# Kernel tuning notes

Measured on AMD Instinct MI355X. Metric: run time of the kernel, lower is better.

## Reference

```python
import jax, jax.numpy as jnp
import numpy as np

B, S, D = 16, 2048, 64
K, M = 8, 2048

def setup_inputs() -> dict:
    key = jax.random.key(0)
    kx, kc = jax.random.split(key)
    x = jax.random.normal(kx, (B, S, D), dtype=jnp.float32)
    # nn.init.uniform_(weight, -1/M, 1/M)
    codebooks = jax.random.uniform(kc, (K, M, D), dtype=jnp.float32,
                                   minval=-1.0 / M, maxval=1.0 / M)
    return {"x": x, "codebooks": codebooks}

def reference(x, codebooks):
    """Residual VQ: sequentially quantize residual against K codebooks.

    x: (B,S,D) float32; codebooks: (K,M,D) float32.
    Returns (quantized (B,S,D), indices (K,B,S) int32).
    Uses squared-distance expansion ||r||^2 - 2 r.c + ||c||^2 (argmin-equivalent
    to torch.norm) to avoid materializing the (B,S,M,D) difference tensor.
    """
    def step(residual, cb):  # residual: (B,S,D), cb: (M,D)
        r2 = jnp.sum(residual * residual, axis=-1, keepdims=True)   # (B,S,1)
        c2 = jnp.sum(cb * cb, axis=-1)                              # (M,)
        cross = jnp.einsum('bsd,md->bsm', residual, cb)             # (B,S,M)
        d2 = r2 - 2.0 * cross + c2                                  # (B,S,M)
        idx = jnp.argmin(d2, axis=-1)                               # (B,S)
        q = cb[idx]                                                 # (B,S,D) gather
        return residual - q, idx

    residual, indices = jax.lax.scan(step, x, codebooks)
    quantized = x - residual
    return quantized, indices
```

## Files before the change

kernel.cpp:

```cpp
#include <hip/hip_runtime.h>


#define BB 16
#define SS 2048
#define DD 64
#define KK 8
#define MM 2048
#define NPTS (BB * SS)
#define QSIZE (NPTS * DD)
#define NCHUNK 8
#define WPB 8
#define PPB 512
#define MCHUNK (MM / NCHUNK)
#define PACKF 16640

__global__ __launch_bounds__(256) void rvq_prep(const float* __restrict__ cb,
                                                float* __restrict__ pack,
                                                unsigned long long* __restrict__ keys) {
#pragma clang fp contract(off)
    const int b = blockIdx.x;
    const int tid = threadIdx.x;
    const float* src = cb + (size_t)b * 16384;
    float* dst = pack + (size_t)b * PACKF;
    for (int i = tid; i < 4096; i += 256)
        *(float4*)&dst[i * 4] = *(const float4*)&src[i * 4];
    const float* row = src + (size_t)tid * DD;
    float r[8];
#pragma unroll
    for (int j = 0; j < 8; ++j) { float v = row[j]; r[j] = v * v; }
#pragma unroll
    for (int i = 8; i < DD; i += 8) {
#pragma unroll
        for (int j = 0; j < 8; ++j) { float v = row[i + j]; float t = v * v; r[j] += t; }
    }
    dst[16384 + tid] = ((r[0] + r[1]) + (r[2] + r[3])) + ((r[4] + r[5]) + (r[6] + r[7]));
    keys[b * 512 + tid] = ~0ULL;
    keys[b * 512 + 256 + tid] = ~0ULL;
}

#define R2K(A, B, C, E) \
    "v_pk_mul_f32 v[92:93], v[" A "], v[" A "]\n\t" \
    "v_pk_add_f32 v[80:81], v[80:81], v[92:93]\n\t" \
    "v_pk_mul_f32 v[92:93], v[" B "], v[" B "]\n\t" \
    "v_pk_add_f32 v[82:83], v[82:83], v[92:93]\n\t" \
    "v_pk_mul_f32 v[92:93], v[" C "], v[" C "]\n\t" \
    "v_pk_add_f32 v[84:85], v[84:85], v[92:93]\n\t" \
    "v_pk_mul_f32 v[92:93], v[" E "], v[" E "]\n\t" \
    "v_pk_add_f32 v[86:87], v[86:87], v[92:93]\n\t"

#define GRP(SA, SB, VA, VB) \
    "v_pk_mul_f32 v[84:85], s[" SA "], v[" VA "]\n\t" \
    "v_pk_mul_f32 v[86:87], s[" SB "], v[" VB "]\n\t" \
    "v_pk_add_f32 v[80:81], v[80:81], v[84:85]\n\t" \
    "v_pk_add_f32 v[82:83], v[82:83], v[86:87]\n\t"

#define GRPL(CA, CB, VA, VB) \
    "v_pk_mul_f32 v[84:85], v[" CA "], v[" VA "]\n\t" \
    "v_pk_mul_f32 v[86:87], v[" CB "], v[" VB "]\n\t" \
    "v_pk_add_f32 v[80:81], v[80:81], v[84:85]\n\t" \
    "v_pk_add_f32 v[82:83], v[82:83], v[86:87]\n\t"

#define SMEM_B_ISSUE \
    "s_add_u32 s15, s14, 0x100\n\t" \
    "s_load_dwordx16 s[16:31], %[pb], s15\n\t" \
    "s_add_u32 s15, s15, 0x40\n\t" \
    "s_load_dwordx16 s[80:95], %[pb], s15\n\t"

#define C2_ISSUE \
    "s_lshr_b32 s15, s14, 6\n\t" \
    "s_add_u32 s15, s15, 0x10008\n\t" \
    "s_min_u32 s15, s15, 0x103f8\n\t" \
    "s_load_dwordx2 s[12:13], %[pb], s15\n\t"

#define SMEM_A_NEXT \
    "s_add_u32 s15, s14, 0x200\n\t" \
    "s_min_u32 s15, s15, 0xfe00\n\t" \
    "s_load_dwordx16 s[32:47], %[pb], s15\n\t" \
    "s_add_u32 s15, s15, 0x40\n\t" \
    "s_load_dwordx16 s[48:63], %[pb], s15\n\t" \
    "s_add_u32 s15, s15, 0x40\n\t" \
    "s_load_dwordx16 s[64:79], %[pb], s15\n\t"

#define EINSM_A \
    "v_pk_mul_f32 v[80:81], s[44:45], v[28:29]\n\t" \
    "v_pk_mul_f32 v[82:83], s[46:47], v[30:31]\n\t" \
    GRP("40:41","42:43","24:25","26:27") \
    GRP("36:37","38:39","20:21","22:23") \
    GRP("32:33","34:35","16:17","18:19") \
    GRP("60:61","62:63","44:45","46:47") \
    GRP("56:57","58:59","40:41","42:43") \
    GRP("52:53","54:55","36:37","38:39") \
    GRP("48:49","50:51","32:33","34:35") \
    GRP("76:77","78:79","60:61","62:63") \
    GRP("72:73","74:75","56:57","58:59") \
    GRP("68:69","70:71","52:53","54:55") \
    GRP("64:65","66:67","48:49","50:51")

#define TAIL_A \
    GRPL("108:109","110:111","76:77","78:79") \
    GRPL("104:105","106:107","72:73","74:75") \
    GRPL("100:101","102:103","68:69","70:71") \
    GRPL("96:97","98:99","64:65","66:67")

#define DS_B \
    "ds_read_b128 v[96:99],   v94 offset:64\n\t" \
    "ds_read_b128 v[100:103], v94 offset:80\n\t" \
    "ds_read_b128 v[104:107], v94 offset:96\n\t" \
    "ds_read_b128 v[108:111], v94 offset:112\n\t" \
    "ds_read_b128 v[112:115], v94 offset:128\n\t" \
    "ds_read_b128 v[116:119], v94 offset:144\n\t" \
    "ds_read_b128 v[120:123], v94 offset:160\n\t" \
    "ds_read_b128 v[124:127], v94 offset:176\n\t"

#define EINSM_B \
    "v_pk_mul_f32 v[80:81], s[28:29], v[28:29]\n\t" \
    "v_pk_mul_f32 v[82:83], s[30:31], v[30:31]\n\t" \
    GRP("24:25","26:27","24:25","26:27") \
    GRP("20:21","22:23","20:21","22:23") \
    GRP("16:17","18:19","16:17","18:19") \
    GRP("92:93","94:95","44:45","46:47") \
    GRP("88:89","90:91","40:41","42:43") \
    GRP("84:85","86:87","36:37","38:39") \
    GRP("80:81","82:83","32:33","34:35")

#define B_B32_THEN_DSA \
    GRPL("108:109","110:111","60:61","62:63") \
    GRPL("104:105","106:107","56:57","58:59") \
    GRPL("100:101","102:103","52:53","54:55") \
    GRPL("96:97","98:99","48:49","50:51") \
    "ds_read_b128 v[96:99],   v94 offset:192\n\t" \
    "ds_read_b128 v[100:103], v94 offset:208\n\t" \
    "ds_read_b128 v[104:107], v94 offset:224\n\t" \
    "ds_read_b128 v[108:111], v94 offset:240\n\t"

#define B_B48 \
    GRPL("124:125","126:127","76:77","78:79") \
    GRPL("120:121","122:123","72:73","74:75") \
    GRPL("116:117","118:119","68:69","70:71") \
    GRPL("112:113","114:115","64:65","66:67") \
    "v_add_u32 v94, 0xc0, v94\n\t"

#define FINX(C2R) \
    "v_add_f32 v92, v80, v81\n\t" \
    "v_add_f32 v93, v82, v83\n\t" \
    "v_add_f32 v92, v92, v93\n\t" \
    "v_fma_f32 v92, v92, -2.0, v88\n\t" \
    "v_add_f32 v92, " C2R ", v92\n\t" \
    "v_cmp_lt_f32 vcc, v92, v89\n\t" \
    "v_cndmask_b32 v89, v89, v92, vcc\n\t" \
    "v_cndmask_b32 v90, v90, v91, vcc\n\t" \
    "v_add_u32 v91, 1, v91\n\t"

__global__ __launch_bounds__(512, 4) void rvq_main(const float* __restrict__ res_in,
                                                   const float* __restrict__ packk,
                                                   unsigned long long* __restrict__ keys) {
#pragma clang fp contract(off)
    const int tid = threadIdx.x;
    const int lane = tid & 63;
    const int wv = __builtin_amdgcn_readfirstlane(tid >> 6);
    const int ch = blockIdx.x & (NCHUNK - 1);
    const int bp = blockIdx.x >> 3;
    const int point = bp * PPB + wv * 64 + lane;

    const int m0 = ch * MCHUNK;
    const float* pbw = packk + (size_t)ch * PACKF;
    const unsigned long long ra = (unsigned long long)(res_in + (size_t)point * DD);

    __shared__ __align__(16) float lds_cb[128 * 48 + 48];
    for (int i = tid; i < 128 * 12; i += PPB) {
        const int q = i / 12;
        const int j = i - q * 12;
        const int row = 2 * q + (j >= 4);
        const int d = (j < 4) ? (48 + 4 * j) : (16 + 4 * j);
        *(float4*)&lds_cb[q * 48 + j * 4] = *(const float4*)(pbw + row * DD + d);
    }
    __syncthreads();
    const unsigned ldsbase = (unsigned)(unsigned long long)(void*)&lds_cb[0];

    float best;
    int bidx;
    asm volatile(
        "global_load_dwordx4 v[16:19], %[ra], off\n\t"
        "global_load_dwordx4 v[20:23], %[ra], off offset:16\n\t"
        "global_load_dwordx4 v[24:27], %[ra], off offset:32\n\t"
        "global_load_dwordx4 v[28:31], %[ra], off offset:48\n\t"
        "global_load_dwordx4 v[32:35], %[ra], off offset:64\n\t"
        "global_load_dwordx4 v[36:39], %[ra], off offset:80\n\t"
        "global_load_dwordx4 v[40:43], %[ra], off offset:96\n\t"
        "global_load_dwordx4 v[44:47], %[ra], off offset:112\n\t"
        "global_load_dwordx4 v[48:51], %[ra], off offset:128\n\t"
        "global_load_dwordx4 v[52:55], %[ra], off offset:144\n\t"
        "global_load_dwordx4 v[56:59], %[ra], off offset:160\n\t"
        "global_load_dwordx4 v[60:63], %[ra], off offset:176\n\t"
        "global_load_dwordx4 v[64:67], %[ra], off offset:192\n\t"
        "global_load_dwordx4 v[68:71], %[ra], off offset:208\n\t"
        "global_load_dwordx4 v[72:75], %[ra], off offset:224\n\t"
        "global_load_dwordx4 v[76:79], %[ra], off offset:240\n\t"
        "s_waitcnt vmcnt(0)\n\t"
        "v_pk_mul_f32 v[80:81], v[16:17], v[16:17]\n\t"
        "v_pk_mul_f32 v[82:83], v[18:19], v[18:19]\n\t"
        "v_pk_mul_f32 v[84:85], v[20:21], v[20:21]\n\t"
        "v_pk_mul_f32 v[86:87], v[22:23], v[22:23]\n\t"
        R2K("24:25", "26:27", "28:29", "30:31")
        R2K("32:33", "34:35", "36:37", "38:39")
        R2K("40:41", "42:43", "44:45", "46:47")
        R2K("48:49", "50:51", "52:53", "54:55")
        R2K("56:57", "58:59", "60:61", "62:63")
        R2K("64:65", "66:67", "68:69", "70:71")
        R2K("72:73", "74:75", "76:77", "78:79")
        "v_add_f32 v92, v80, v81\n\t"
        "v_add_f32 v93, v82, v83\n\t"
        "v_add_f32 v92, v92, v93\n\t"
        "v_add_f32 v93, v84, v85\n\t"
        "v_add_f32 v88, v86, v87\n\t"
        "v_add_f32 v93, v93, v88\n\t"
        "v_add_f32 v88, v92, v93\n\t"
        "v_mov_b32 v89, 0x7f800000\n\t"
        "v_mov_b32 v90, 0\n\t"
        "v_mov_b32 v91, %[m0]\n\t"
        "v_mov_b32 v94, %[lb]\n\t"
        "s_mov_b32 s14, 0\n\t"
        "s_load_dwordx16 s[32:47], %[pb], 0x0\n\t"
        "s_load_dwordx16 s[48:63], %[pb], 0x40\n\t"
        "s_load_dwordx16 s[64:79], %[pb], 0x80\n\t"
        "s_load_dwordx2 s[12:13], %[pb], 0x10000\n\t"
        "ds_read_b128 v[96:99],   v94\n\t"
        "ds_read_b128 v[100:103], v94 offset:16\n\t"
        "ds_read_b128 v[104:107], v94 offset:32\n\t"
        "ds_read_b128 v[108:111], v94 offset:48\n\t"
        "Ltop_%=:\n\t"
        "s_waitcnt lgkmcnt(0)\n\t"
        "v_mov_b32 v15, s12\n\t"
        "v_mov_b32 v95, s13\n\t"
        SMEM_B_ISSUE
        C2_ISSUE
        EINSM_A
        TAIL_A
        DS_B
        FINX("v15")
        "s_waitcnt lgkmcnt(0)\n\t"
        SMEM_A_NEXT
        EINSM_B
        B_B32_THEN_DSA
        B_B48
        FINX("v95")
        "s_add_u32 s14, s14, 0x200\n\t"
        "s_cmp_lg_u32 s14, 0x10000\n\t"
        "s_cbranch_scc1 Ltop_%=\n\t"
        "s_waitcnt lgkmcnt(0)\n\t"
        "v_mov_b32 %[ob], v89\n\t"
        "v_mov_b32 %[oi], v90\n\t"
        : [ob] "=v"(best), [oi] "=v"(bidx)
        : [ra] "v"(ra), [pb] "s"(pbw), [m0] "v"(m0), [lb] "v"(ldsbase)
        : "vcc", "scc",
          "s12","s13","s14","s15",
          "s16","s17","s18","s19","s20","s21","s22","s23","s24","s25","s26","s27",
          "s28","s29","s30","s31","s32","s33","s34","s35","s36","s37","s38","s39",
          "s40","s41","s42","s43","s44","s45","s46","s47","s48","s49","s50","s51",
          "s52","s53","s54","s55","s56","s57","s58","s59","s60","s61","s62","s63",
          "s64","s65","s66","s67","s68","s69","s70","s71","s72","s73","s74","s75",
          "s76","s77","s78","s79","s80","s81","s82","s83","s84","s85","s86","s87",
          "s88","s89","s90","s91","s92","s93","s94","s95",
          "v15",
          "v16","v17","v18","v19","v20","v21","v22","v23","v24","v25","v26","v27",
          "v28","v29","v30","v31","v32","v33","v34","v35","v36","v37","v38","v39",
          "v40","v41","v42","v43","v44","v45","v46","v47","v48","v49","v50","v51",
          "v52","v53","v54","v55","v56","v57","v58","v59","v60","v61","v62","v63",
          "v64","v65","v66","v67","v68","v69","v70","v71","v72","v73","v74","v75",
          "v76","v77","v78","v79","v80","v81","v82","v83","v84","v85","v86","v87",
          "v88","v89","v90","v91","v92","v93","v94","v95","v96","v97","v98","v99",
          "v100","v101","v102","v103","v104","v105","v106","v107","v108","v109",
          "v110","v111","v112","v113","v114","v115","v116","v117","v118","v119",
          "v120","v121","v122","v123","v124","v125","v126","v127");

    unsigned long long key =
        ((unsigned long long)__float_as_uint(best) << 32) | (unsigned int)bidx;
    atomicMin(&keys[point], key);
}

__global__ __launch_bounds__(256) void rvq_update(const float* __restrict__ res_in,
                                                  float* __restrict__ res_out,
                                                  const float* __restrict__ x,
                                                  const float* __restrict__ cbk,
                                                  unsigned long long* __restrict__ keys,
                                                  float* __restrict__ idx_out,
                                                  int last) {
#pragma clang fp contract(off)
    __shared__ unsigned long long sk[4];
    const int tid = threadIdx.x;
    const int e = blockIdx.x * 256 + tid;
    const int p0 = blockIdx.x * 4;
    if (tid < 4) {
        unsigned long long k = keys[p0 + tid];
        sk[tid] = k;
        keys[p0 + tid] = ~0ULL;
        idx_out[p0 + tid] = (float)(unsigned int)k;
    }
    __syncthreads();
    const int pi = tid >> 6;
    const int d = tid & 63;
    const int m = (int)(unsigned int)sk[pi];
    const float r = res_in[e] - cbk[(size_t)m * DD + d];
    if (last) res_out[e] = x[e] - r;
    else      res_out[e] = r;
}

extern "C" void kernel_launch(void* const* d_in, const int* in_sizes, int n_in,
                              void* d_out, int out_size, void* d_ws, size_t ws_size,
                              hipStream_t stream) {
    const float* x  = (const float*)d_in[0];
    const float* cb = (const float*)d_in[1];

    float* out = (float*)d_out;
    float* quant = out;
    float* idx_out = out + QSIZE;

    float* res1 = (float*)d_ws;
    unsigned long long* keys =
        (unsigned long long*)(res1 + (size_t)QSIZE);
    float* pack = (float*)(keys + NPTS);
    float* R[2] = { quant, res1 };

    rvq_prep<<<KK * NCHUNK, 256, 0, stream>>>(cb, pack, keys);

    for (int k = 0; k < KK; ++k) {
        const float* rin = (k == 0) ? x : R[(k - 1) & 1];
        const int last = (k == KK - 1);
        float* rout = last ? quant : R[k & 1];
        rvq_main<<<(NPTS / PPB) * NCHUNK, PPB, 0, stream>>>(
            rin,
            pack + (size_t)k * NCHUNK * PACKF,
            keys);
        rvq_update<<<QSIZE / 256, 256, 0, stream>>>(
            rin, rout, x,
            cb + (size_t)k * MM * DD,
            keys,
            idx_out + (size_t)k * NPTS,
            last);
    }
}
```

Before: 1.282 ms.

## Fuse residual update into main kernel via last-block-done counter

Removes the separate rvq_update launch per codebook stage. Each main block bumps a per-point-group atomic counter after publishing its atomicMin key, and the last of the NCHUNK chunk blocks reads the final keys, writes indices, and computes the new residual (or the final quantized output) for its 512 points. This saves 8 kernel launches and the extra pass over the residual, but adds fences, an atomic counter, and a serialized tail where only one block in each group does the update, with each thread handling a full row instead of coalesced per-element access.

```diff
diff --git a/kernel.cpp b/kernel.cpp
--- a/kernel.cpp
+++ b/kernel.cpp
@@ -13,10 +13,12 @@
 #define PPB 512
 #define MCHUNK (MM / NCHUNK)
 #define PACKF 16640
+#define NGRP (NPTS / PPB)
 
 __global__ __launch_bounds__(256) void rvq_prep(const float* __restrict__ cb,
                                                 float* __restrict__ pack,
-                                                unsigned long long* __restrict__ keys) {
+                                                unsigned long long* __restrict__ keys,
+                                                unsigned* __restrict__ cnt) {
 #pragma clang fp contract(off)
     const int b = blockIdx.x;
     const int tid = threadIdx.x;
@@ -36,6 +38,7 @@
     dst[16384 + tid] = ((r[0] + r[1]) + (r[2] + r[3])) + ((r[4] + r[5]) + (r[6] + r[7]));
     keys[b * 512 + tid] = ~0ULL;
     keys[b * 512 + 256 + tid] = ~0ULL;
+    if (b == 0 && tid < NGRP) cnt[tid] = 0;
 }
 
 #define R2K(A, B, C, E) \
@@ -152,8 +155,13 @@
     "v_add_u32 v91, 1, v91\n\t"
 
 __global__ __launch_bounds__(512, 4) void rvq_main(const float* __restrict__ res_in,
+                                                   float* __restrict__ res_out,
+                                                   const float* __restrict__ xg,
                                                    const float* __restrict__ packk,
-                                                   unsigned long long* __restrict__ keys) {
+                                                   unsigned long long* __restrict__ keys,
+                                                   unsigned* __restrict__ cnt,
+                                                   float* __restrict__ idx_out,
+                                                   int last) {
 #pragma clang fp contract(off)
     const int tid = threadIdx.x;
     const int lane = tid & 63;
@@ -167,6 +175,7 @@
     const unsigned long long ra = (unsigned long long)(res_in + (size_t)point * DD);
 
     __shared__ __align__(16) float lds_cb[128 * 48 + 48];
+    __shared__ unsigned s_rank;
     for (int i = tid; i < 128 * 12; i += PPB) {
         const int q = i / 12;
         const int j = i - q * 12;
@@ -276,33 +285,46 @@
     unsigned long long key =
         ((unsigned long long)__float_as_uint(best) << 32) | (unsigned int)bidx;
     atomicMin(&keys[point], key);
-}
-
-__global__ __launch_bounds__(256) void rvq_update(const float* __restrict__ res_in,
-                                                  float* __restrict__ res_out,
-                                                  const float* __restrict__ x,
-                                                  const float* __restrict__ cbk,
-                                                  unsigned long long* __restrict__ keys,
-                                                  float* __restrict__ idx_out,
-                                                  int last) {
-#pragma clang fp contract(off)
-    __shared__ unsigned long long sk[4];
-    const int tid = threadIdx.x;
-    const int e = blockIdx.x * 256 + tid;
-    const int p0 = blockIdx.x * 4;
-    if (tid < 4) {
-        unsigned long long k = keys[p0 + tid];
-        sk[tid] = k;
-        keys[p0 + tid] = ~0ULL;
-        idx_out[p0 + tid] = (float)(unsigned int)k;
+
+    __threadfence();
+    __syncthreads();
+    if (tid == 0) s_rank = atomicAdd(&cnt[bp], 1u);
+    __syncthreads();
+    if (s_rank == NCHUNK - 1) {
+        __threadfence();
+        const int p = bp * PPB + tid;
+        const unsigned long long kk = atomicMin(&keys[p], ~0ULL);
+        const int m = (int)(unsigned int)kk;
+        keys[p] = ~0ULL;
+        idx_out[p] = (float)m;
+        const float4* crow = (const float4*)(packk + (size_t)(m >> 8) * PACKF
+                                                   + (size_t)(m & 255) * DD);
+        const float4* rrow = (const float4*)(res_in + (size_t)p * DD);
+        float4* orow = (float4*)(res_out + (size_t)p * DD);
+        if (last) {
+            const float4* xrow = (const float4*)(xg + (size_t)p * DD);
+#pragma unroll 4
+            for (int j = 0; j < 16; ++j) {
+                float4 rv = rrow[j], cv = crow[j], xv = xrow[j], ov;
+                ov.x = xv.x - (rv.x - cv.x);
+                ov.y = xv.y - (rv.y - cv.y);
+                ov.z = xv.z - (rv.z - cv.z);
+                ov.w = xv.w - (rv.w - cv.w);
+                orow[j] = ov;
+            }
+        } else {
+#pragma unroll 4
+            for (int j = 0; j < 16; ++j) {
+                float4 rv = rrow[j], cv = crow[j], ov;
+                ov.x = rv.x - cv.x;
+                ov.y = rv.y - cv.y;
+                ov.z = rv.z - cv.z;
+                ov.w = rv.w - cv.w;
+                orow[j] = ov;
+            }
+        }
+        if (tid == 0) cnt[bp] = 0;
     }
-    __syncthreads();
-    const int pi = tid >> 6;
-    const int d = tid & 63;
-    const int m = (int)(unsigned int)sk[pi];
-    const float r = res_in[e] - cbk[(size_t)m * DD + d];
-    if (last) res_out[e] = x[e] - r;
-    else      res_out[e] = r;
 }
 
 extern "C" void kernel_launch(void* const* d_in, const int* in_sizes, int n_in,
@@ -319,22 +341,19 @@
     unsigned long long* keys =
         (unsigned long long*)(res1 + (size_t)QSIZE);
     float* pack = (float*)(keys + NPTS);
+    unsigned* cnt = (unsigned*)(pack + (size_t)KK * NCHUNK * PACKF);
     float* R[2] = { quant, res1 };
 
-    rvq_prep<<<KK * NCHUNK, 256, 0, stream>>>(cb, pack, keys);
+    rvq_prep<<<KK * NCHUNK, 256, 0, stream>>>(cb, pack, keys, cnt);
 
     for (int k = 0; k < KK; ++k) {
         const float* rin = (k == 0) ? x : R[(k - 1) & 1];
         const int last = (k == KK - 1);
         float* rout = last ? quant : R[k & 1];
         rvq_main<<<(NPTS / PPB) * NCHUNK, PPB, 0, stream>>>(
-            rin,
+            rin, rout, x,
             pack + (size_t)k * NCHUNK * PACKF,
-            keys);
-        rvq_update<<<QSIZE / 256, 256, 0, stream>>>(
-            rin, rout, x,
-            cb + (size_t)k * MM * DD,
-            keys,
+            keys, cnt,
             idx_out + (size_t)k * NPTS,
             last);
     }
```

Result: slower. 2.139 ms (+66.9%).
